# Kernel optimization log

Hardware: AMD Instinct MI355X
Metric: run time of the kernel (lower is better)

## Reference

```python
import math
import jax, jax.numpy as jnp
import numpy as np

B, S, E, H = 2, 2048, 1024, 16
DK = E // H

def setup_inputs() -> dict:
    key = jax.random.key(0)
    ks = jax.random.split(key, 12)
    sc = 1.0 / math.sqrt(E)
    return {
        "x": jax.random.normal(ks[0], (B, S, E), jnp.float32),
        "kv": jax.random.normal(ks[1], (B, S, E), jnp.float32),
        "mask": jax.random.randint(ks[2], (B, S), 0, 2, jnp.int32),
        "attn_bias": jax.random.normal(ks[3], (B, S, S), jnp.float32),
        "WQ_w": jax.random.normal(ks[4], (E, E), jnp.float32) * sc,
        "WQ_b": jnp.zeros((E,), jnp.float32),
        "WK_w": jax.random.normal(ks[5], (E, E), jnp.float32) * sc,
        "WK_b": jnp.zeros((E,), jnp.float32),
        "WV_w": jax.random.normal(ks[6], (E, E), jnp.float32) * sc,
        "WV_b": jnp.zeros((E,), jnp.float32),
        "WO_w": jax.random.normal(ks[7], (E, E), jnp.float32) * sc,
        "WO_b": jnp.zeros((E,), jnp.float32),
    }

def reference(x, kv, mask, attn_bias, WQ_w, WQ_b, WK_w, WK_b, WV_w, WV_b, WO_w, WO_b):
    b, sq, _ = x.shape
    sk = kv.shape[1]
    # projections, split heads: [B,S,E] -> [B,H,S,DK]
    Q = (x @ WQ_w.T + WQ_b).reshape(b, sq, H, DK).transpose(0, 2, 1, 3)
    K = (kv @ WK_w.T + WK_b).reshape(b, sk, H, DK).transpose(0, 2, 1, 3)
    V = (kv @ WV_w.T + WV_b).reshape(b, sk, H, DK).transpose(0, 2, 1, 3)
    # scores [B,H,Sq,Sk]
    T = jnp.einsum('bhqd,bhkd->bhqk', Q, K) / math.sqrt(DK)
    T = T + attn_bias[:, None, :, :]  # 3D bias broadcast over heads
    m2 = jnp.einsum('bi,bj->bij', mask.astype(T.dtype), mask.astype(T.dtype))
    T = jnp.where(m2[:, None, :, :] == 0, jnp.asarray(-1e9, T.dtype), T)
    A = jax.nn.softmax(T, axis=-1)
    out = jnp.einsum('bhqk,bhkd->bhqd', A, V)  # [B,H,Sq,DK]
    out = out.transpose(0, 2, 1, 3).reshape(b, sq, E)
    return out @ WO_w.T + WO_b
```

## Files before the change

### kernel.cpp

```cpp
#include <hip/hip_runtime.h>

#define DEV static __device__ __forceinline__

typedef __attribute__((ext_vector_type(8))) __bf16 bf16x8;
typedef __attribute__((ext_vector_type(4))) float f32x4;

constexpr int CB = 2;
constexpr int CS = 2048;
constexpr int CE = 1024;
constexpr int CH = 16;
constexpr int CD = 64;
constexpr float LOG2E = 1.44269504f;

DEV unsigned short f2bf(float x) {
  unsigned int u = __float_as_uint(x);
  u += 0x7fffu + ((u >> 16) & 1u);
  return (unsigned short)(u >> 16);
}

DEV f32x4 mfma32(bf16x8 a, bf16x8 b, f32x4 c) {
  return __builtin_amdgcn_mfma_f32_16x16x32_bf16(a, b, c, 0, 0, 0);
}

DEV unsigned int cvtpk(float lo, float hi) {
  unsigned int r;
  asm("v_cvt_pk_bf16_f32 %0, %1, %2" : "=v"(r) : "v"(lo), "v"(hi));
  return r;
}

DEV float exp2r(float x) {
#if __has_builtin(__builtin_amdgcn_exp2f)
  return __builtin_amdgcn_exp2f(x);
#else
  float r; asm("v_exp_f32 %0, %1" : "=v"(r) : "v"(x)); return r;
#endif
}

DEV f32x4 unpk(unsigned int a, unsigned int b) {
  f32x4 r;
  r[0] = __uint_as_float(a << 16);
  r[1] = __uint_as_float(a & 0xffff0000u);
  r[2] = __uint_as_float(b << 16);
  r[3] = __uint_as_float(b & 0xffff0000u);
  return r;
}

DEV void stage16(const void* g, void* l) {
  __builtin_amdgcn_global_load_lds(
      (const __attribute__((address_space(1))) unsigned int*)g,
      (__attribute__((address_space(3))) unsigned int*)l, 16, 0, 0);
}

__global__ __launch_bounds__(256) void wcvt_all(const float* __restrict__ w0,
                                                const float* __restrict__ w1,
                                                const float* __restrict__ w2,
                                                const float* __restrict__ w3,
                                                unsigned short* __restrict__ out) {
  const long WE = (long)CE * CE;
  const long i = ((long)blockIdx.x * 256 + threadIdx.x) * 8;
  const int wi = (int)(i >> 20);
  const float* src = wi == 0 ? w0 : wi == 1 ? w1 : wi == 2 ? w2 : w3;
  const long off = i & (WE - 1);
  float4 a = *reinterpret_cast<const float4*>(src + off);
  float4 b = *reinterpret_cast<const float4*>(src + off + 4);
  uint4 v;
  v.x = cvtpk(a.x, a.y); v.y = cvtpk(a.z, a.w);
  v.z = cvtpk(b.x, b.y); v.w = cvtpk(b.z, b.w);
  *reinterpret_cast<uint4*>(out + i) = v;
}

DEV void mbias_body512(long idx, const float* __restrict__ bias, const int* __restrict__ mask,
                       unsigned short* __restrict__ mb16) {
  const int b = (int)(idx >> 22);
  const int q = (int)((idx >> 11) & (CS - 1));
  const int k0 = (int)(idx & (CS - 1));
  const bool mq = mask[b * CS + q] != 0;
  const int4 mk0 = *reinterpret_cast<const int4*>(mask + b * CS + k0);
  const int4 mk1 = *reinterpret_cast<const int4*>(mask + b * CS + k0 + 4);
  const float4 b0 = *reinterpret_cast<const float4*>(bias + idx);
  const float4 b1 = *reinterpret_cast<const float4*>(bias + idx + 4);
  const float NEG = -1e9f * LOG2E;
  float v[8];
  if (mq) {
    v[0] = (mk0.x != 0) ? b0.x * LOG2E : NEG;
    v[1] = (mk0.y != 0) ? b0.y * LOG2E : NEG;
    v[2] = (mk0.z != 0) ? b0.z * LOG2E : NEG;
    v[3] = (mk0.w != 0) ? b0.w * LOG2E : NEG;
    v[4] = (mk1.x != 0) ? b1.x * LOG2E : NEG;
    v[5] = (mk1.y != 0) ? b1.y * LOG2E : NEG;
    v[6] = (mk1.z != 0) ? b1.z * LOG2E : NEG;
    v[7] = (mk1.w != 0) ? b1.w * LOG2E : NEG;
  } else {
#pragma unroll
    for (int j = 0; j < 8; j++) v[j] = 0.f;
  }
  uint4 o;
  o.x = cvtpk(v[0], v[1]); o.y = cvtpk(v[2], v[3]);
  o.z = cvtpk(v[4], v[5]); o.w = cvtpk(v[6], v[7]);
  *reinterpret_cast<uint4*>(mb16 + idx) = o;
}

__global__ __launch_bounds__(512) void gemm_qkv(const float* __restrict__ xf,
                                                const float* __restrict__ kvf,
                                                const unsigned short* __restrict__ Wall,
                                                const float* __restrict__ bq,
                                                const float* __restrict__ bk,
                                                const float* __restrict__ bv,
                                                unsigned short* __restrict__ Qb,
                                                const float* __restrict__ bias,
                                                const int* __restrict__ mask,
                                                unsigned short* __restrict__ mb16) {
  __shared__ __align__(16) unsigned char ldsA[32768];
  __shared__ __align__(16) unsigned char ldsB[32768];
  const int bx = blockIdx.x;
  const int tid = threadIdx.x;
  if (bx >= 192) {
    const long base = ((long)(bx - 192) * 512 + tid) * 8;
    const long stride = 256L * 512 * 8;
#pragma unroll
    for (int itr = 0; itr < 8; itr++)
      mbias_body512(base + (long)itr * stride, bias, mask, mb16);
    return;
  }
  const long NE = (long)CB * CS * CE;
  const long WE = (long)CE * CE;
  const int mx = bx & 15, ny = bx >> 4;
  const int which = ny >> 2;
  const int n0 = (ny & 3) * 256;
  const int m0 = mx * 256;
  const float* Ax = which == 0 ? xf : kvf;
  const unsigned char* Bb = (const unsigned char*)(Wall + (long)which * WE);
  const float* bq_ = which == 0 ? bq : which == 1 ? bk : bv;

  const int lane = tid & 63, w = tid >> 6;
  const int wr = w >> 2, wc = w & 3;
  const int g = lane >> 4, rr = lane & 15;

  const int srow = tid >> 2;
  const int ecol = ((tid & 3) * 8) ^ (((tid >> 5) & 1) * 16);
  const float* afp0 = Ax + (long)(m0 + srow) * CE + ecol;
  const float* afp1 = Ax + (long)(m0 + 128 + srow) * CE + ecol;
  const float* afb0 = afp0;
  const float* afb1 = afp1;
  const int scsw = ((tid & 3) * 16) ^ (((tid >> 5) & 1) << 5);
  const unsigned char* bpR0 = Bb + ((long)(n0 + srow) * CE) * 2 + scsw;
  const unsigned char* bpR1 = Bb + ((long)(n0 + 128 + srow) * CE) * 2 + scsw;

  const int cswz = (g * 16) ^ (((rr >> 3) & 1) << 5);
  const unsigned char* rbA = ldsA + wr * 8192 + rr * 64 + cswz;
  const unsigned char* rbB = ldsB + wc * 4096 + rr * 64 + cswz;

  f32x4 acc[8][4] = {};
  float4 afr0, afr1, afr2, afr3;

  auto loadA = [&](bool junk) {
    const float* p0 = junk ? afb0 : afp0;
    const float* p1 = junk ? afb1 : afp1;
    afr0 = *reinterpret_cast<const float4*>(p0);
    afr1 = *reinterpret_cast<const float4*>(p0 + 4);
    afr2 = *reinterpret_cast<const float4*>(p1);
    afr3 = *reinterpret_cast<const float4*>(p1 + 4);
    if (!junk) { afp0 += 32; afp1 += 32; }
  };
  auto writeA = [&](int buf) {
    uint4 w0v, w1v;
    w0v.x = cvtpk(afr0.x, afr0.y); w0v.y = cvtpk(afr0.z, afr0.w);
    w0v.z = cvtpk(afr1.x, afr1.y); w0v.w = cvtpk(afr1.z, afr1.w);
    w1v.x = cvtpk(afr2.x, afr2.y); w1v.y = cvtpk(afr2.z, afr2.w);
    w1v.z = cvtpk(afr3.x, afr3.y); w1v.w = cvtpk(afr3.z, afr3.w);
    *reinterpret_cast<uint4*>(ldsA + buf * 16384 + tid * 16) = w0v;
    *reinterpret_cast<uint4*>(ldsA + buf * 16384 + 8192 + tid * 16) = w1v;
  };
  auto stB = [&](int buf) {
    stage16(bpR0, ldsB + buf * 16384 + w * 1024);
    stage16(bpR1, ldsB + buf * 16384 + 8192 + w * 1024);
    bpR0 += 64; bpR1 += 64;
  };

  loadA(false);
  stB(0);
  asm volatile("s_waitcnt vmcnt(2)" ::: "memory");
  writeA(0);
  loadA(false);
  stB(1);
  asm volatile("s_waitcnt vmcnt(6)" ::: "memory");
  asm volatile("s_waitcnt lgkmcnt(0)" ::: "memory");
  __builtin_amdgcn_s_barrier();

  auto group = [&](int buf, bool junk) {
    bf16x8 ar[4], br[4];
#pragma unroll
    for (int ii = 0; ii < 4; ii++)
      ar[ii] = *reinterpret_cast<const bf16x8*>(rbA + buf * 16384 + ii * 1024);
#pragma unroll
    for (int j = 0; j < 4; j++)
      br[j] = *reinterpret_cast<const bf16x8*>(rbB + buf * 16384 + j * 1024);
    asm volatile("s_waitcnt vmcnt(2)" ::: "memory");
    writeA(buf ^ 1);
    loadA(junk);
    asm volatile("s_waitcnt lgkmcnt(0)" ::: "memory");
    __builtin_amdgcn_sched_barrier(0);
    __builtin_amdgcn_s_setprio(1);
#pragma unroll
    for (int ii = 0; ii < 4; ii++)
#pragma unroll
      for (int j = 0; j < 4; j++)
        acc[ii][j] = mfma32(ar[ii], br[j], acc[ii][j]);
    __builtin_amdgcn_s_setprio(0);
    __builtin_amdgcn_s_barrier();
#pragma unroll
    for (int ii = 0; ii < 4; ii++)
      ar[ii] = *reinterpret_cast<const bf16x8*>(rbA + buf * 16384 + 4096 + ii * 1024);
    stB(buf);
    asm volatile("s_waitcnt lgkmcnt(0)" ::: "memory");
    __builtin_amdgcn_sched_barrier(0);
    __builtin_amdgcn_s_setprio(1);
#pragma unroll
    for (int ii = 0; ii < 4; ii++)
#pragma unroll
      for (int j = 0; j < 4; j++)
        acc[4 + ii][j] = mfma32(ar[ii], br[j], acc[4 + ii][j]);
    __builtin_amdgcn_s_setprio(0);
    asm volatile("s_waitcnt vmcnt(6)" ::: "memory");
    __builtin_amdgcn_s_barrier();
  };

#pragma unroll 1
  for (int it = 0; it < 16; ++it) {
    group(0, it == 15);
    group(1, it == 15);
  }
  asm volatile("s_waitcnt vmcnt(0)" ::: "memory");

  const float scale = which == 0 ? 0.125f * LOG2E : 1.0f;
#pragma unroll
  for (int i = 0; i < 8; i++) {
#pragma unroll
    for (int j = 0; j < 4; j++) {
      const int colg = n0 + wc * 64 + j * 16 + rr;
      const float bvv = bq_[colg];
      if (which == 2) {
        const int rowbase = m0 + wr * 128 + i * 16 + g * 4;
        const int bb = rowbase >> 11, s = rowbase & 2047;
        const int hh = colg >> 6, d = colg & 63;
        uint2 val;
        val.x = (unsigned int)f2bf(acc[i][j][0] + bvv) | ((unsigned int)f2bf(acc[i][j][1] + bvv) << 16);
        val.y = (unsigned int)f2bf(acc[i][j][2] + bvv) | ((unsigned int)f2bf(acc[i][j][3] + bvv) << 16);
        *reinterpret_cast<uint2*>(Qb + 2 * NE + ((long)((bb * CH + hh) * CD + d)) * CS + s) = val;
      } else {
        unsigned short* outp = Qb + (long)which * NE;
#pragma unroll
        for (int r = 0; r < 4; r++) {
          const int row = m0 + wr * 128 + i * 16 + g * 4 + r;
          outp[(long)row * CE + colg] = f2bf((acc[i][j][r] + bvv) * scale);
        }
      }
    }
  }
}

__global__ __launch_bounds__(256) void gemm_wo(const unsigned short* __restrict__ A,
                                               const unsigned short* __restrict__ W,
                                               const float* __restrict__ bias,
                                               float* __restrict__ out) {
  __shared__ __align__(16) unsigned short As[128 * 64];
  __shared__ __align__(16) unsigned short Bs[64 * 64];
  const int tid = threadIdx.x;
  const int lane = tid & 63, wave = tid >> 6;
  const int wm = (wave >> 1) * 64, wn = (wave & 1) * 32;
  const int g = lane >> 4, rr = lane & 15;
  const int m0 = blockIdx.x * 128, n0 = blockIdx.y * 64;
  const int K = CE;
  f32x4 acc[4][2] = {};

  for (int k0 = 0; k0 < K; k0 += 64) {
#pragma unroll
    for (int t = 0; t < 4; t++) {
      const int u = t * 256 + tid;
      const int row = u >> 3, ce = (u & 7) * 8;
      stage16(A + (long)(m0 + row) * K + k0 + ce, (char*)As + (t * 256 + (tid & 192)) * 16);
    }
#pragma unroll
    for (int t = 0; t < 2; t++) {
      const int u = t * 256 + tid;
      const int row = u >> 3, ce = (u & 7) * 8;
      stage16(W + (long)(n0 + row) * K + k0 + ce, (char*)Bs + (t * 256 + (tid & 192)) * 16);
    }
    __syncthreads();
#pragma unroll
    for (int kk = 0; kk < 2; kk++) {
      bf16x8 af[4], bfr[2];
#pragma unroll
      for (int i = 0; i < 4; i++)
        af[i] = *reinterpret_cast<const bf16x8*>(&As[(wm + i * 16 + rr) * 64 + kk * 32 + g * 8]);
#pragma unroll
      for (int j = 0; j < 2; j++)
        bfr[j] = *reinterpret_cast<const bf16x8*>(&Bs[(wn + j * 16 + rr) * 64 + kk * 32 + g * 8]);
#pragma unroll
      for (int i = 0; i < 4; i++)
#pragma unroll
        for (int j = 0; j < 2; j++)
          acc[i][j] = mfma32(af[i], bfr[j], acc[i][j]);
    }
    __syncthreads();
  }

#pragma unroll
  for (int i = 0; i < 4; i++)
#pragma unroll
    for (int j = 0; j < 2; j++) {
      const int colg = n0 + wn + j * 16 + rr;
      const float bvv = bias[colg];
#pragma unroll
      for (int r = 0; r < 4; r++) {
        const int row = m0 + wm + i * 16 + g * 4 + r;
        out[(long)row * CE + colg] = acc[i][j][r] + bvv;
      }
    }
}

__global__ __launch_bounds__(256, 2) void attn_kernel(const unsigned short* __restrict__ Qb,
                                                      const unsigned short* __restrict__ Kb,
                                                      const unsigned short* __restrict__ Vtw,
                                                      const unsigned short* __restrict__ mb16,
                                                      const int* __restrict__ mask,
                                                      unsigned short* __restrict__ AO) {
  __shared__ __align__(16) unsigned char lds[65536];
  const int h = blockIdx.x, qt = blockIdx.y, b = blockIdx.z;
  const int tid = threadIdx.x;
  const int lane = tid & 63, w = tid >> 6;
  const int g = lane >> 4, c = lane & 15;
  const int qbase = qt * 128 + w * 32;

  bf16x8 qf[2][2];
#pragma unroll
  for (int qb = 0; qb < 2; qb++) {
    const unsigned short* Qrow = Qb + ((long)b * CS + qbase + qb * 16 + c) * CE + h * CD;
    qf[qb][0] = *reinterpret_cast<const bf16x8*>(Qrow + g * 8);
    qf[qb][1] = *reinterpret_cast<const bf16x8*>(Qrow + 32 + g * 8);
    if (mask[b * CS + qbase + qb * 16 + c] == 0) {
      qf[qb][0] = bf16x8{}; qf[qb][1] = bf16x8{};
    }
  }

  const unsigned char *kg[4], *vg[4];
  {
    const unsigned char* Ksrc = (const unsigned char*)(Kb + (long)b * CS * CE + h * CD);
    const unsigned char* Vsrc = (const unsigned char*)(Vtw + (long)(b * CH + h) * CD * CS);
    const int rr8 = lane >> 3;
    const int csw = ((lane & 7) << 4) ^ (rr8 << 4);
#pragma unroll
    for (int t = 0; t < 4; t++) {
      const int krow = t * 32 + w * 8 + rr8;
      const int key = (krow & 96) + ((krow >> 2) & 3) * 8 + ((krow >> 4) & 1) * 4 + (krow & 3);
      kg[t] = Ksrc + (long)key * (CE * 2) + csw;
      const int vrow = (t & 1) * 32 + w * 8 + rr8;
      vg[t] = Vsrc + (long)vrow * (CS * 2) + (t >> 1) * 128 + csw;
    }
  }
  const int sw = (c & 7) << 4;
  const unsigned char* rb0 = lds + c * 128 + ((g * 16) ^ sw);
  const unsigned char* rb1 = lds + c * 128 + ((64 + g * 16) ^ sw);

  const unsigned short* mbp0 = mb16 + ((long)b * CS + qbase + c) * CS + g * 8;
  const unsigned short* mbp1 = mb16 + ((long)b * CS + qbase + 16 + c) * CS + g * 8;

  f32x4 o[2][4] = {};
  f32x4 lsum4[2] = {};
  uint4 mbr[2][4];

  auto stage = [&](int bo) {
    unsigned char* kbuf = lds + bo;
    unsigned char* vbuf = lds + bo + 16384;
#pragma unroll
    for (int t = 0; t < 4; t++) {
      stage16(kg[t], kbuf + t * 4096 + w * 1024);
      stage16(vg[t], vbuf + (t >> 1) * 8192 + (t & 1) * 4096 + w * 1024);
      kg[t] += 128 * CE * 2;
      vg[t] += 128 * 2;
    }
  };
  auto load_mb = [&](bool adv) {
#pragma unroll
    for (int kb = 0; kb < 4; kb++) {
      mbr[0][kb] = *reinterpret_cast<const uint4*>(mbp0 + kb * 32);
      mbr[1][kb] = *reinterpret_cast<const uint4*>(mbp1 + kb * 32);
    }
    if (adv) { mbp0 += 128; mbp1 += 128; }
  };

  auto compute = [&](int bo, bool adv) {
    f32x4 sf[2][8];
    __builtin_amdgcn_s_setprio(1);
#pragma unroll
    for (int cb = 0; cb < 8; cb++) {
      const bf16x8 kf0 = *reinterpret_cast<const bf16x8*>(rb0 + bo + cb * 2048);
      const bf16x8 kf1 = *reinterpret_cast<const bf16x8*>(rb1 + bo + cb * 2048);
#pragma unroll
      for (int qb = 0; qb < 2; qb++) {
        const uint4 m = mbr[qb][cb >> 1];
        const f32x4 ci = (cb & 1) ? unpk(m.z, m.w) : unpk(m.x, m.y);
        f32x4 t = mfma32(kf0, qf[qb][0], ci);
        sf[qb][cb] = mfma32(kf1, qf[qb][1], t);
      }
    }
    __builtin_amdgcn_s_setprio(0);
    load_mb(adv);
    uint4 pw[2][4];
#pragma unroll
    for (int qb = 0; qb < 2; qb++)
#pragma unroll
      for (int kb = 0; kb < 4; kb++)
#pragma unroll
        for (int half = 0; half < 2; half++) {
          const int cb = 2 * kb + half;
          f32x4 pv;
          pv[0] = exp2r(sf[qb][cb][0]);
          pv[1] = exp2r(sf[qb][cb][1]);
          pv[2] = exp2r(sf[qb][cb][2]);
          pv[3] = exp2r(sf[qb][cb][3]);
          lsum4[qb] = lsum4[qb] + pv;
          if (half == 0) { pw[qb][kb].x = cvtpk(pv[0], pv[1]); pw[qb][kb].y = cvtpk(pv[2], pv[3]); }
          else           { pw[qb][kb].z = cvtpk(pv[0], pv[1]); pw[qb][kb].w = cvtpk(pv[2], pv[3]); }
        }
    __builtin_amdgcn_s_setprio(1);
#pragma unroll
    for (int nb = 0; nb < 4; nb++) {
#pragma unroll
      for (int kb = 0; kb < 4; kb++) {
        const unsigned char* rbx = (kb & 1) ? rb1 : rb0;
        const bf16x8 vf = *reinterpret_cast<const bf16x8*>(
            rbx + bo + 16384 + (kb >> 1) * 8192 + nb * 2048);
#pragma unroll
        for (int qb = 0; qb < 2; qb++)
          o[qb][nb] = mfma32(vf, __builtin_bit_cast(bf16x8, pw[qb][kb]), o[qb][nb]);
      }
    }
    __builtin_amdgcn_s_setprio(0);
  };

  stage(0);
  load_mb(true);
  stage(32768);

#pragma unroll 1
  for (int it = 0; it < 8; ++it) {
    asm volatile("s_waitcnt vmcnt(16)" ::: "memory");
    __builtin_amdgcn_s_barrier();
    __builtin_amdgcn_sched_barrier(0);
    compute(0, it < 7);
    __builtin_amdgcn_sched_barrier(0);
    __builtin_amdgcn_s_barrier();
    stage(0);
    asm volatile("s_waitcnt vmcnt(16)" ::: "memory");
    __builtin_amdgcn_s_barrier();
    __builtin_amdgcn_sched_barrier(0);
    compute(32768, it < 7);
    __builtin_amdgcn_sched_barrier(0);
    __builtin_amdgcn_s_barrier();
    stage(32768);
  }

#pragma unroll
  for (int qb = 0; qb < 2; qb++) {
    float lsum = (lsum4[qb][0] + lsum4[qb][1]) + (lsum4[qb][2] + lsum4[qb][3]);
    lsum += __shfl_xor(lsum, 16, 64);
    lsum += __shfl_xor(lsum, 32, 64);
    const float linv = 1.0f / lsum;
    unsigned short* Orow = AO + ((long)b * CS + qbase + qb * 16 + c) * CE + h * CD;
#pragma unroll
    for (int nb = 0; nb < 4; nb++) {
      uint2 val;
      val.x = (unsigned int)f2bf(o[qb][nb][0] * linv) | ((unsigned int)f2bf(o[qb][nb][1] * linv) << 16);
      val.y = (unsigned int)f2bf(o[qb][nb][2] * linv) | ((unsigned int)f2bf(o[qb][nb][3] * linv) << 16);
      *reinterpret_cast<uint2*>(Orow + nb * 16 + g * 4) = val;
    }
  }
  asm volatile("s_waitcnt vmcnt(0)" ::: "memory");
}

extern "C" void kernel_launch(void* const* d_in, const int* in_sizes, int n_in,
                              void* d_out, int out_size, void* d_ws, size_t ws_size,
                              hipStream_t stream) {
  (void)in_sizes; (void)n_in; (void)out_size; (void)ws_size;
  const float* x    = (const float*)d_in[0];
  const float* kv   = (const float*)d_in[1];
  const int*   mask = (const int*)d_in[2];
  const float* ab   = (const float*)d_in[3];
  const float* WQw  = (const float*)d_in[4];
  const float* WQb  = (const float*)d_in[5];
  const float* WKw  = (const float*)d_in[6];
  const float* WKb  = (const float*)d_in[7];
  const float* WVw  = (const float*)d_in[8];
  const float* WVb  = (const float*)d_in[9];
  const float* WOw  = (const float*)d_in[10];
  const float* WOb  = (const float*)d_in[11];
  float* out = (float*)d_out;

  const long NE = (long)CB * CS * CE;
  const long WE = (long)CE * CE;
  unsigned short* ws  = (unsigned short*)d_ws;
  unsigned short* wqb = ws;
  unsigned short* wob = wqb + 3 * WE;
  unsigned short* Qb  = wob + WE;
  unsigned short* AO  = Qb + 3 * NE;
  unsigned short* mb16 = AO + NE;

  wcvt_all<<<(int)((4 * WE) / 2048), 256, 0, stream>>>(WQw, WKw, WVw, WOw, wqb);

  gemm_qkv<<<dim3(192 + 256), 512, 0, stream>>>(x, kv, wqb, WQb, WKb, WVb, Qb,
                                                ab, mask, mb16);

  attn_kernel<<<dim3(CH, CS / 128, CB), 256, 0, stream>>>(
      Qb, Qb + NE, Qb + 2 * NE, mb16, mask, AO);

  gemm_wo<<<dim3(32, 16), 256, 0, stream>>>(AO, wob, WOb, out);
}
```

Measured before the change: 128.6 us.

## Fuse weight fp32-to-bf16 conversion into QKV GEMM and drop separate convert kernel

```diff
diff --git a/kernel.cpp b/kernel.cpp
--- a/kernel.cpp
+++ b/kernel.cpp
@@ -49,24 +49,6 @@
   __builtin_amdgcn_global_load_lds(
       (const __attribute__((address_space(1))) unsigned int*)g,
       (__attribute__((address_space(3))) unsigned int*)l, 16, 0, 0);
-}
-
-__global__ __launch_bounds__(256) void wcvt_all(const float* __restrict__ w0,
-                                                const float* __restrict__ w1,
-                                                const float* __restrict__ w2,
-                                                const float* __restrict__ w3,
-                                                unsigned short* __restrict__ out) {
-  const long WE = (long)CE * CE;
-  const long i = ((long)blockIdx.x * 256 + threadIdx.x) * 8;
-  const int wi = (int)(i >> 20);
-  const float* src = wi == 0 ? w0 : wi == 1 ? w1 : wi == 2 ? w2 : w3;
-  const long off = i & (WE - 1);
-  float4 a = *reinterpret_cast<const float4*>(src + off);
-  float4 b = *reinterpret_cast<const float4*>(src + off + 4);
-  uint4 v;
-  v.x = cvtpk(a.x, a.y); v.y = cvtpk(a.z, a.w);
-  v.z = cvtpk(b.x, b.y); v.w = cvtpk(b.z, b.w);
-  *reinterpret_cast<uint4*>(out + i) = v;
 }
 
 DEV void mbias_body512(long idx, const float* __restrict__ bias, const int* __restrict__ mask,
@@ -100,36 +82,56 @@
   *reinterpret_cast<uint4*>(mb16 + idx) = o;
 }
 
+DEV void wcvt1_body(long i, const float* __restrict__ src, unsigned short* __restrict__ out) {
+  float4 a = *reinterpret_cast<const float4*>(src + i);
+  float4 b = *reinterpret_cast<const float4*>(src + i + 4);
+  uint4 v;
+  v.x = cvtpk(a.x, a.y); v.y = cvtpk(a.z, a.w);
+  v.z = cvtpk(b.x, b.y); v.w = cvtpk(b.z, b.w);
+  *reinterpret_cast<uint4*>(out + i) = v;
+}
+
 __global__ __launch_bounds__(512) void gemm_qkv(const float* __restrict__ xf,
                                                 const float* __restrict__ kvf,
-                                                const unsigned short* __restrict__ Wall,
+                                                const float* __restrict__ WQw,
+                                                const float* __restrict__ WKw,
+                                                const float* __restrict__ WVw,
                                                 const float* __restrict__ bq,
                                                 const float* __restrict__ bk,
                                                 const float* __restrict__ bv,
                                                 unsigned short* __restrict__ Qb,
                                                 const float* __restrict__ bias,
                                                 const int* __restrict__ mask,
-                                                unsigned short* __restrict__ mb16) {
+                                                unsigned short* __restrict__ mb16,
+                                                const float* __restrict__ WOw,
+                                                unsigned short* __restrict__ wob) {
   __shared__ __align__(16) unsigned char ldsA[32768];
   __shared__ __align__(16) unsigned char ldsB[32768];
   const int bx = blockIdx.x;
   const int tid = threadIdx.x;
   if (bx >= 192) {
-    const long base = ((long)(bx - 192) * 512 + tid) * 8;
-    const long stride = 256L * 512 * 8;
-#pragma unroll
-    for (int itr = 0; itr < 8; itr++)
-      mbias_body512(base + (long)itr * stride, bias, mask, mb16);
+    if (bx < 448) {
+      const long base = ((long)(bx - 192) * 512 + tid) * 8;
+      const long stride = 256L * 512 * 8;
+#pragma unroll
+      for (int itr = 0; itr < 8; itr++)
+        mbias_body512(base + (long)itr * stride, bias, mask, mb16);
+    } else {
+      const long base = ((long)(bx - 448) * 512 + tid) * 8;
+      const long stride = 32L * 512 * 8;
+#pragma unroll
+      for (int itr = 0; itr < 8; itr++)
+        wcvt1_body(base + (long)itr * stride, WOw, wob);
+    }
     return;
   }
   const long NE = (long)CB * CS * CE;
-  const long WE = (long)CE * CE;
   const int mx = bx & 15, ny = bx >> 4;
   const int which = ny >> 2;
   const int n0 = (ny & 3) * 256;
   const int m0 = mx * 256;
   const float* Ax = which == 0 ? xf : kvf;
-  const unsigned char* Bb = (const unsigned char*)(Wall + (long)which * WE);
+  const float* Bw = which == 0 ? WQw : which == 1 ? WKw : WVw;
   const float* bq_ = which == 0 ? bq : which == 1 ? bk : bv;
 
   const int lane = tid & 63, w = tid >> 6;
@@ -142,9 +144,10 @@
   const float* afp1 = Ax + (long)(m0 + 128 + srow) * CE + ecol;
   const float* afb0 = afp0;
   const float* afb1 = afp1;
-  const int scsw = ((tid & 3) * 16) ^ (((tid >> 5) & 1) << 5);
-  const unsigned char* bpR0 = Bb + ((long)(n0 + srow) * CE) * 2 + scsw;
-  const unsigned char* bpR1 = Bb + ((long)(n0 + 128 + srow) * CE) * 2 + scsw;
+  const float* bfp0 = Bw + (long)(n0 + srow) * CE + ecol;
+  const float* bfp1 = Bw + (long)(n0 + 128 + srow) * CE + ecol;
+  const float* bfb0 = bfp0;
+  const float* bfb1 = bfp1;
 
   const int cswz = (g * 16) ^ (((rr >> 3) & 1) << 5);
   const unsigned char* rbA = ldsA + wr * 8192 + rr * 64 + cswz;
@@ -152,6 +155,7 @@
 
   f32x4 acc[8][4] = {};
   float4 afr0, afr1, afr2, afr3;
+  float4 bfr0, bfr1, bfr2, bfr3;
 
   auto loadA = [&](bool junk) {
     const float* p0 = junk ? afb0 : afp0;
@@ -162,6 +166,15 @@
     afr3 = *reinterpret_cast<const float4*>(p1 + 4);
     if (!junk) { afp0 += 32; afp1 += 32; }
   };
+  auto loadB = [&](bool junk) {
+    const float* p0 = junk ? bfb0 : bfp0;
+    const float* p1 = junk ? bfb1 : bfp1;
+    bfr0 = *reinterpret_cast<const float4*>(p0);
+    bfr1 = *reinterpret_cast<const float4*>(p0 + 4);
+    bfr2 = *reinterpret_cast<const float4*>(p1);
+    bfr3 = *reinterpret_cast<const float4*>(p1 + 4);
+    if (!junk) { bfp0 += 32; bfp1 += 32; }
+  };
   auto writeA = [&](int buf) {
     uint4 w0v, w1v;
     w0v.x = cvtpk(afr0.x, afr0.y); w0v.y = cvtpk(afr0.z, afr0.w);
@@ -171,19 +184,24 @@
     *reinterpret_cast<uint4*>(ldsA + buf * 16384 + tid * 16) = w0v;
     *reinterpret_cast<uint4*>(ldsA + buf * 16384 + 8192 + tid * 16) = w1v;
   };
-  auto stB = [&](int buf) {
-    stage16(bpR0, ldsB + buf * 16384 + w * 1024);
-    stage16(bpR1, ldsB + buf * 16384 + 8192 + w * 1024);
-    bpR0 += 64; bpR1 += 64;
+  auto writeB = [&](int buf) {
+    uint4 w0v, w1v;
+    w0v.x = cvtpk(bfr0.x, bfr0.y); w0v.y = cvtpk(bfr0.z, bfr0.w);
+    w0v.z = cvtpk(bfr1.x, bfr1.y); w0v.w = cvtpk(bfr1.z, bfr1.w);
+    w1v.x = cvtpk(bfr2.x, bfr2.y); w1v.y = cvtpk(bfr2.z, bfr2.w);
+    w1v.z = cvtpk(bfr3.x, bfr3.y); w1v.w = cvtpk(bfr3.z, bfr3.w);
+    *reinterpret_cast<uint4*>(ldsB + buf * 16384 + tid * 16) = w0v;
+    *reinterpret_cast<uint4*>(ldsB + buf * 16384 + 8192 + tid * 16) = w1v;
   };
 
   loadA(false);
-  stB(0);
-  asm volatile("s_waitcnt vmcnt(2)" ::: "memory");
+  loadB(false);
+  asm volatile("s_waitcnt vmcnt(4)" ::: "memory");
   writeA(0);
   loadA(false);
-  stB(1);
-  asm volatile("s_waitcnt vmcnt(6)" ::: "memory");
+  asm volatile("s_waitcnt vmcnt(4)" ::: "memory");
+  writeB(0);
+  loadB(false);
   asm volatile("s_waitcnt lgkmcnt(0)" ::: "memory");
   __builtin_amdgcn_s_barrier();
 
@@ -195,7 +213,7 @@
 #pragma unroll
     for (int j = 0; j < 4; j++)
       br[j] = *reinterpret_cast<const bf16x8*>(rbB + buf * 16384 + j * 1024);
-    asm volatile("s_waitcnt vmcnt(2)" ::: "memory");
+    asm volatile("s_waitcnt vmcnt(4)" ::: "memory");
     writeA(buf ^ 1);
     loadA(junk);
     asm volatile("s_waitcnt lgkmcnt(0)" ::: "memory");
@@ -211,7 +229,9 @@
 #pragma unroll
     for (int ii = 0; ii < 4; ii++)
       ar[ii] = *reinterpret_cast<const bf16x8*>(rbA + buf * 16384 + 4096 + ii * 1024);
-    stB(buf);
+    asm volatile("s_waitcnt vmcnt(4)" ::: "memory");
+    writeB(buf ^ 1);
+    loadB(junk);
     asm volatile("s_waitcnt lgkmcnt(0)" ::: "memory");
     __builtin_amdgcn_sched_barrier(0);
     __builtin_amdgcn_s_setprio(1);
@@ -221,7 +241,6 @@
       for (int j = 0; j < 4; j++)
         acc[4 + ii][j] = mfma32(ar[ii], br[j], acc[4 + ii][j]);
     __builtin_amdgcn_s_setprio(0);
-    asm volatile("s_waitcnt vmcnt(6)" ::: "memory");
     __builtin_amdgcn_s_barrier();
   };
 
@@ -500,16 +519,13 @@
   const long NE = (long)CB * CS * CE;
   const long WE = (long)CE * CE;
   unsigned short* ws  = (unsigned short*)d_ws;
-  unsigned short* wqb = ws;
-  unsigned short* wob = wqb + 3 * WE;
+  unsigned short* wob = ws + 3 * WE;
   unsigned short* Qb  = wob + WE;
   unsigned short* AO  = Qb + 3 * NE;
   unsigned short* mb16 = AO + NE;
 
-  wcvt_all<<<(int)((4 * WE) / 2048), 256, 0, stream>>>(WQw, WKw, WVw, WOw, wqb);
-
-  gemm_qkv<<<dim3(192 + 256), 512, 0, stream>>>(x, kv, wqb, WQb, WKb, WVb, Qb,
-                                                ab, mask, mb16);
+  gemm_qkv<<<dim3(192 + 256 + 32), 512, 0, stream>>>(
+      x, kv, WQw, WKw, WVw, WQb, WKb, WVb, Qb, ab, mask, mb16, WOw, wob);
 
   attn_kernel<<<dim3(CH, CS / 128, CB), 256, 0, stream>>>(
       Qb, Qb + NE, Qb + 2 * NE, mb16, mask, AO);
```

Result: faster. 118.8 us (-7.6%).
